# Kernel optimization log

Hardware: AMD Instinct MI355X
Metric: run time of the kernel (lower is better)

The kernel has to match this reference:

```python
import jax, jax.numpy as jnp
import numpy as np

N_NODES = 100000
N_EDGES = 3200000
N_GRAPHS = 256
FEAT = 128
HIDDEN = 128
N_CLASSES = 10


def setup_inputs() -> dict:
    key = jax.random.key(0)
    ks = jax.random.split(key, 12)
    x = jax.random.normal(ks[0], (N_NODES, FEAT), dtype=jnp.float32)
    edge_index = jax.random.randint(ks[1], (2, N_EDGES), 0, N_NODES, dtype=jnp.int64)
    batch = jnp.sort(jax.random.randint(ks[2], (N_NODES,), 0, N_GRAPHS, dtype=jnp.int64))
    s = 0.05
    return {
        "x": x,
        "edge_index": edge_index,
        "batch": batch,
        "W1": jax.random.normal(ks[3], (FEAT, HIDDEN), dtype=jnp.float32) * s,
        "b1": jnp.zeros((HIDDEN,), dtype=jnp.float32),
        "W2": jax.random.normal(ks[4], (HIDDEN, HIDDEN), dtype=jnp.float32) * s,
        "b2": jnp.zeros((HIDDEN,), dtype=jnp.float32),
        "W3": jax.random.normal(ks[5], (HIDDEN, HIDDEN), dtype=jnp.float32) * s,
        "b3": jnp.zeros((HIDDEN,), dtype=jnp.float32),
        "lin1_w": jax.random.normal(ks[6], (HIDDEN, HIDDEN), dtype=jnp.float32) * s,
        "lin1_b": jnp.zeros((HIDDEN,), dtype=jnp.float32),
        "lin2_w": jax.random.normal(ks[7], (HIDDEN, N_CLASSES), dtype=jnp.float32) * s,
        "lin2_b": jnp.zeros((N_CLASSES,), dtype=jnp.float32),
    }


def _gcn_norm(edge_index, n_nodes):
    # PyG GCNConv default: add self-loops, symmetric normalization.
    src = jnp.concatenate([edge_index[0], jnp.arange(n_nodes, dtype=edge_index.dtype)])
    dst = jnp.concatenate([edge_index[1], jnp.arange(n_nodes, dtype=edge_index.dtype)])
    deg = jax.ops.segment_sum(jnp.ones_like(dst, dtype=jnp.float32), dst, num_segments=n_nodes)
    dis = jnp.where(deg > 0, jax.lax.rsqrt(jnp.maximum(deg, 1.0)), 0.0)
    norm = dis[src] * dis[dst]  # [E + N]
    return src, dst, norm


def _gcn_conv(x, src, dst, norm, W, b, n_nodes):
    h = x @ W                               # [N, H]
    msg = h[src] * norm[:, None]            # gather + scale, [E+N, H]
    out = jax.ops.segment_sum(msg, dst, num_segments=n_nodes)  # scatter-add
    return out + b


def reference(x, edge_index, batch, W1, b1, W2, b2, W3, b3, lin1_w, lin1_b, lin2_w, lin2_b):
    n = x.shape[0]
    src, dst, norm = _gcn_norm(edge_index, n)
    h = jax.nn.relu(_gcn_conv(x, src, dst, norm, W1, b1, n))
    h = jax.nn.relu(_gcn_conv(h, src, dst, norm, W2, b2, n))
    h = jax.nn.relu(_gcn_conv(h, src, dst, norm, W3, b3, n))
    # global mean pool over graphs
    sums = jax.ops.segment_sum(h, batch, num_segments=N_GRAPHS)
    cnts = jax.ops.segment_sum(jnp.ones((n,), dtype=h.dtype), batch, num_segments=N_GRAPHS)
    g = sums / jnp.maximum(cnts, 1.0)[:, None]
    g = jax.nn.relu(g @ lin1_w + lin1_b)
    # dropout p=0.5 is identity at inference
    return g @ lin2_w + lin2_b
```

## Files before the change

### kernel.cpp

```cpp
#include <hip/hip_runtime.h>
#include <hip/hip_fp16.h>

#define FEAT 128
#define CHUNK 8192
#define BSH 7
#define CAP 6144
#define RSTRIDE 784

#define QS  16.0f
#define QSI 0.0625f

typedef _Float16 half8 __attribute__((ext_vector_type(8)));
typedef float floatx4 __attribute__((ext_vector_type(4)));
typedef float floatx2 __attribute__((ext_vector_type(2)));

__device__ __forceinline__ unsigned int enc8x4(float a, float b, float c, float d) {
  unsigned int r = __builtin_amdgcn_cvt_pk_fp8_f32(a, b, 0u, false);
  return __builtin_amdgcn_cvt_pk_fp8_f32(c, d, r, true);
}
__device__ __forceinline__ void acc8(unsigned int w, float* a) {
  floatx2 v0 = __builtin_amdgcn_cvt_pk_f32_fp8(w, false);
  floatx2 v1 = __builtin_amdgcn_cvt_pk_f32_fp8(w, true);
  a[0] += v0.x; a[1] += v0.y; a[2] += v1.x; a[3] += v1.y;
}


__global__ __launch_bounds__(256) void sort_prep_kernel(
    const int* __restrict__ ei, int E, int nchunks, int nbuk,
    int* __restrict__ pairs, int* __restrict__ runs,
    const float* __restrict__ W1, const float* __restrict__ W2,
    const float* __restrict__ W3, _Float16* __restrict__ P1,
    _Float16* __restrict__ P2, _Float16* __restrict__ P3,
    unsigned char* __restrict__ qA, unsigned char* __restrict__ qB, int N) {
  __shared__ int lhist[1024];
  __shared__ int lofs[1024];
  __shared__ int lcur[1024];
  __shared__ int tsum[256];
  __shared__ int stage[CHUNK];
  int t = threadIdx.x;
  if ((int)blockIdx.x >= nchunks) {
    int b = blockIdx.x - nchunks;
    if (b == 24) {
      if (t < 16) ((unsigned long long*)(qA + (size_t)N * FEAT))[t] = 0ull;
      else if (t < 32) ((unsigned long long*)(qB + (size_t)N * FEAT))[t - 16] = 0ull;
      return;
    }
    const float* W = (b < 8) ? W1 : (b < 16) ? W2 : W3;
    _Float16* P = (b < 8) ? P1 : (b < 16) ? P2 : P3;
    int e = (b & 7) * 256 + t;
    int l = e & 63;
    int ks = (e >> 6) & 3;
    int tn = e >> 8;
    int n = tn * 16 + (l & 15);
    int k0 = ks * 32 + (l >> 4) * 8;
    half8 v;
#pragma unroll
    for (int j = 0; j < 8; ++j) v[j] = (_Float16)W[(k0 + j) * 128 + n];
    *(half8*)(P + (size_t)e * 8) = v;
    return;
  }
  int c = blockIdx.x;
  int e0 = c * CHUNK;
  int e1 = e0 + CHUNK; if (e1 > E) e1 = E;
  int cnt = e1 - e0;
#pragma unroll
  for (int u = 0; u < 4; ++u) lhist[t + u * 256] = 0;
  __syncthreads();
  for (int j = e0 + t; j < e1; j += 256) atomicAdd(&lhist[ei[E + j] >> BSH], 1);
  __syncthreads();
  int a0 = lhist[4 * t], a1 = lhist[4 * t + 1];
  int a2 = lhist[4 * t + 2], a3 = lhist[4 * t + 3];
  int s = ((a0 + a1) + (a2 + a3));
  tsum[t] = s;
  __syncthreads();
  for (int o = 1; o < 256; o <<= 1) {
    int x = (t >= o) ? tsum[t - o] : 0;
    __syncthreads();
    tsum[t] += x;
    __syncthreads();
  }
  int base = tsum[t] - s;
  lofs[4 * t] = base;       lcur[4 * t] = base;
  lofs[4 * t + 1] = base + a0;           lcur[4 * t + 1] = base + a0;
  lofs[4 * t + 2] = base + a0 + a1;      lcur[4 * t + 2] = base + a0 + a1;
  lofs[4 * t + 3] = base + a0 + a1 + a2; lcur[4 * t + 3] = base + a0 + a1 + a2;
  __syncthreads();
  for (int k = t; k < nbuk; k += 256) runs[(size_t)c * RSTRIDE + k] = lofs[k];
  if (t == 0) runs[(size_t)c * RSTRIDE + nbuk] = cnt;
  for (int j = e0 + t; j < e1; j += 256) {
    int sv = ei[j];
    int d = ei[E + j];
    int p = atomicAdd(&lcur[d >> BSH], 1);
    stage[p] = sv | ((d & 127) << 24);
  }
  __syncthreads();
  for (int j = t; j < cnt; j += 256) pairs[e0 + j] = stage[j];
}

__global__ __launch_bounds__(256) void bucket_csr_kernel(
    const int* __restrict__ pairs, const int* __restrict__ runs, int nchunks,
    int nbuk, int2* __restrict__ row_se, float* __restrict__ dis,
    int* __restrict__ col, int N) {
  __shared__ int rs[512], rl[512], ro[512];
  __shared__ int cnt[128], sc[128];
  __shared__ int stage[CAP];
  int b = blockIdx.x, t = threadIdx.x;
  for (int c = t; c < 512; c += 256) {
    int s0 = 0, len = 0;
    if (c < nchunks) {
      const int* rr = runs + (size_t)c * RSTRIDE;
      s0 = rr[b];
      len = rr[b + 1] - s0;
    }
    rs[c] = s0; rl[c] = len;
  }
  if (t < 128) cnt[t] = 0;
  __syncthreads();
  ro[t] = rl[t]; ro[t + 256] = rl[t + 256];
  __syncthreads();
  for (int o = 1; o < 512; o <<= 1) {
    int v0 = (t >= o) ? ro[t - o] : 0;
    int v1 = (t + 256 >= o) ? ro[t + 256 - o] : 0;
    __syncthreads();
    ro[t] += v0; ro[t + 256] += v1;
    __syncthreads();
  }
  int ce = ro[511];
  int y0 = ro[t] - rl[t];
  int y1 = ro[t + 256] - rl[t + 256];
  __syncthreads();
  ro[t] = y0; ro[t + 256] = y1;
  __syncthreads();
  int colbase = b * CAP;
  bool fits = ce <= CAP;
  if (fits) {
    for (int c = t; c < nchunks; c += 256) {
      int gs = c * CHUNK + rs[c];
      int base = ro[c];
      int len = rl[c];
      for (int j = 0; j < len; ++j) {
        int p = pairs[gs + j];
        stage[base + j] = p;
        atomicAdd(&cnt[((unsigned)p) >> 24], 1);
      }
    }
  } else {
    for (int c = t; c < nchunks; c += 256) {
      int gs = c * CHUNK + rs[c];
      for (int j = 0; j < rl[c]; ++j)
        atomicAdd(&cnt[((unsigned)pairs[gs + j]) >> 24], 1);
    }
  }
  __syncthreads();
  int v = 0, excl = 0;
  if (t < 128) { v = cnt[t]; sc[t] = v; }
  __syncthreads();
  for (int o = 1; o < 128; o <<= 1) {
    int x = (t >= o && t < 128) ? sc[t - o] : 0;
    __syncthreads();
    if (t < 128) sc[t] += x;
    __syncthreads();
  }
  if (t < 128) {
    excl = sc[t] - v;
    int node = b * 128 + t;
    if (node < N) {
      row_se[node] = make_int2(colbase + excl, colbase + excl + v);
      dis[node] = rsqrtf((float)(v + 1));
    }
    cnt[t] = excl;
  }
  __syncthreads();
  if (fits) {
    for (int j = t; j < ce; j += 256) {
      int p = stage[j];
      int loc = atomicAdd(&cnt[((unsigned)p) >> 24], 1);
      col[colbase + loc] = (p & 0xFFFFFF) << 7;
    }
  } else {
    for (int c = t; c < nchunks; c += 256) {
      int gs = c * CHUNK + rs[c];
      for (int j = 0; j < rl[c]; ++j) {
        int p = pairs[gs + j];
        int loc = atomicAdd(&cnt[((unsigned)p) >> 24], 1);
        if (loc < CAP) col[colbase + loc] = (p & 0xFFFFFF) << 7;
      }
    }
  }
}


__global__ __launch_bounds__(256) void mm1_kernel(
    const float* __restrict__ Av, const _Float16* __restrict__ Wpk,
    const float* __restrict__ scale, unsigned char* __restrict__ C, int N) {
  int t = threadIdx.x;
  int wave = t >> 6, lane = t & 63;
  int quad = lane >> 4, nidx = lane & 15;
  int m0 = blockIdx.x * 64 + wave * 16;
  int arow = m0 + nidx;
  bool avalid = arow < N;
  floatx4 acc[8];
#pragma unroll
  for (int tn = 0; tn < 8; ++tn) acc[tn] = (floatx4){0.f, 0.f, 0.f, 0.f};
#pragma unroll
  for (int ks = 0; ks < 4; ++ks) {
    half8 x = {};
    if (avalid) {
      const float* p = Av + (size_t)arow * 128 + ks * 32 + quad * 8;
      float4 f0 = *(const float4*)p;
      float4 f1 = *(const float4*)(p + 4);
      x[0] = (_Float16)f0.x; x[1] = (_Float16)f0.y;
      x[2] = (_Float16)f0.z; x[3] = (_Float16)f0.w;
      x[4] = (_Float16)f1.x; x[5] = (_Float16)f1.y;
      x[6] = (_Float16)f1.z; x[7] = (_Float16)f1.w;
    }
#pragma unroll
    for (int tn = 0; tn < 8; ++tn) {
      half8 wfrag = *(const half8*)(Wpk + ((size_t)((tn * 4 + ks) * 64 + lane)) * 8);
      acc[tn] = __builtin_amdgcn_mfma_f32_16x16x32_f16(wfrag, x, acc[tn], 0, 0, 0);
    }
  }
  if (avalid) {
    float s = scale[arow] * QS;
#pragma unroll
    for (int tn = 0; tn < 8; ++tn) {
      unsigned int r = enc8x4(acc[tn][0] * s, acc[tn][1] * s,
                              acc[tn][2] * s, acc[tn][3] * s);
      *(unsigned int*)(C + (size_t)arow * 128 + tn * 16 + quad * 4) = r;
    }
  }
}

__global__ __launch_bounds__(256) void agg_fuse_kernel(
    const unsigned char* __restrict__ hs_in, const int2* __restrict__ row_se,
    const int* __restrict__ col, const float* __restrict__ dis,
    const float* __restrict__ bias, const _Float16* __restrict__ Wpk,
    unsigned char* __restrict__ hs_out, int N) {
  __shared__ _Float16 Xs[32][136];
  int t = threadIdx.x;
  int wave = t >> 6, lane = t & 63;
  int lin = lane & 7;
  int nl = wave * 8 + (lane >> 3);
  int node = blockIdx.x * 32 + nl;
  bool valid = node < N;
  int lin16 = lin * 16;
  int zoff = N << 7;
  float a[16];
#pragma unroll
  for (int j = 0; j < 16; ++j) a[j] = 0.f;
  int selfoff = (valid ? (node << 7) : zoff) + lin16;
  uint4 s0 = *(const uint4*)(hs_in + (unsigned)selfoff);
  acc8(s0.x, a); acc8(s0.y, a + 4); acc8(s0.z, a + 8); acc8(s0.w, a + 12);
  int2 se = valid ? row_se[node] : make_int2(0, 0);
  int i = se.x, e = se.y;
  while (__any(i < e)) {
    int c[8];
#pragma unroll
    for (int u = 0; u < 8; ++u) {
      int idx = i + u;
      c[u] = (idx < e) ? col[idx] : zoff;
    }
    uint4 r[8];
#pragma unroll
    for (int u = 0; u < 8; ++u)
      r[u] = *(const uint4*)(hs_in + (unsigned)(c[u] + lin16));
#pragma unroll
    for (int u = 0; u < 8; ++u) {
      acc8(r[u].x, a);     acc8(r[u].y, a + 4);
      acc8(r[u].z, a + 8); acc8(r[u].w, a + 12);
    }
    i += 8;
  }
  float d = valid ? dis[node] * QSI : 0.f;
  const float* bp = bias + lin16;
  half8 hx0, hx1;
#pragma unroll
  for (int j = 0; j < 8; ++j) {
    float o0 = valid ? fmaxf(fmaf(d, a[j], bp[j]), 0.f) : 0.f;
    float o1 = valid ? fmaxf(fmaf(d, a[j + 8], bp[j + 8]), 0.f) : 0.f;
    hx0[j] = (_Float16)o0;
    hx1[j] = (_Float16)o1;
  }
  *(half8*)&Xs[nl][lin16] = hx0;
  *(half8*)&Xs[nl][lin16 + 8] = hx1;
  __syncthreads();
  int quad = lane >> 4, nidx = lane & 15;
  int ntile = wave >> 1;
  int f0 = (wave & 1) * 4;
  floatx4 acc[4];
#pragma unroll
  for (int f = 0; f < 4; ++f) acc[f] = (floatx4){0.f, 0.f, 0.f, 0.f};
#pragma unroll
  for (int ks = 0; ks < 4; ++ks) {
    half8 x = *(const half8*)&Xs[ntile * 16 + nidx][ks * 32 + quad * 8];
#pragma unroll
    for (int f = 0; f < 4; ++f) {
      half8 wf = *(const half8*)(Wpk + ((size_t)(((f0 + f) * 4 + ks) * 64 + lane)) * 8);
      acc[f] = __builtin_amdgcn_mfma_f32_16x16x32_f16(wf, x, acc[f], 0, 0, 0);
    }
  }
  int onode = blockIdx.x * 32 + ntile * 16 + nidx;
  if (onode < N) {
    float sc = dis[onode] * QS;
#pragma unroll
    for (int f = 0; f < 4; ++f) {
      unsigned int rq = enc8x4(acc[f][0] * sc, acc[f][1] * sc,
                               acc[f][2] * sc, acc[f][3] * sc);
      *(unsigned int*)(hs_out + (size_t)onode * 128 + (f0 + f) * 16 + quad * 4) = rq;
    }
  }
}

__global__ __launch_bounds__(256) void agg_kernel(
    const unsigned char* __restrict__ hs, const int2* __restrict__ row_se,
    const int* __restrict__ col, const float* __restrict__ dis,
    const float* __restrict__ bias, _Float16* __restrict__ out, int N) {
  int t = threadIdx.x;
  int wave = t >> 6, lane = t & 63;
  int lin = lane & 7;
  int nl = wave * 8 + (lane >> 3);
  int node = blockIdx.x * 32 + nl;
  bool valid = node < N;
  int lin16 = lin * 16;
  int zoff = N << 7;
  float a[16];
#pragma unroll
  for (int j = 0; j < 16; ++j) a[j] = 0.f;
  int selfoff = (valid ? (node << 7) : zoff) + lin16;
  uint4 s0 = *(const uint4*)(hs + (unsigned)selfoff);
  acc8(s0.x, a); acc8(s0.y, a + 4); acc8(s0.z, a + 8); acc8(s0.w, a + 12);
  int2 se = valid ? row_se[node] : make_int2(0, 0);
  int i = se.x, e = se.y;
  while (__any(i < e)) {
    int c[8];
#pragma unroll
    for (int u = 0; u < 8; ++u) {
      int idx = i + u;
      c[u] = (idx < e) ? col[idx] : zoff;
    }
    uint4 r[8];
#pragma unroll
    for (int u = 0; u < 8; ++u)
      r[u] = *(const uint4*)(hs + (unsigned)(c[u] + lin16));
#pragma unroll
    for (int u = 0; u < 8; ++u) {
      acc8(r[u].x, a);     acc8(r[u].y, a + 4);
      acc8(r[u].z, a + 8); acc8(r[u].w, a + 12);
    }
    i += 8;
  }
  if (valid) {
    float d = dis[node] * QSI;
    const float* bp = bias + lin16;
    half8 hx0, hx1;
#pragma unroll
    for (int j = 0; j < 8; ++j) {
      hx0[j] = (_Float16)fmaxf(fmaf(d, a[j], bp[j]), 0.f);
      hx1[j] = (_Float16)fmaxf(fmaf(d, a[j + 8], bp[j + 8]), 0.f);
    }
    *(half8*)(out + (size_t)node * FEAT + lin16) = hx0;
    *(half8*)(out + (size_t)node * FEAT + lin16 + 8) = hx1;
  }
}

__global__ __launch_bounds__(128) void head_kernel(
    const __half* __restrict__ h, const int* __restrict__ batch,
    const float* __restrict__ l1w, const float* __restrict__ l1b,
    const float* __restrict__ l2w, const float* __restrict__ l2b,
    float* __restrict__ out, int N, int C) {
  __shared__ float row[128];
  __shared__ float row2[128];
  int grp = blockIdx.x, t = threadIdx.x;
  int lo = 0, hi = N;
  while (lo < hi) { int m = (lo + hi) >> 1; if (batch[m] < grp) lo = m + 1; else hi = m; }
  int start = lo;
  hi = N;
  while (lo < hi) { int m = (lo + hi) >> 1; if (batch[m] <= grp) lo = m + 1; else hi = m; }
  int end = lo;
  float a0 = 0.f, a1 = 0.f, a2 = 0.f, a3 = 0.f;
  int i = start;
  for (; i + 4 <= end; i += 4) {
    a0 += __half2float(h[(size_t)i * 128 + t]);
    a1 += __half2float(h[(size_t)(i + 1) * 128 + t]);
    a2 += __half2float(h[(size_t)(i + 2) * 128 + t]);
    a3 += __half2float(h[(size_t)(i + 3) * 128 + t]);
  }
  for (; i < end; ++i) a0 += __half2float(h[(size_t)i * 128 + t]);
  float sum = (a0 + a1) + (a2 + a3);
  float cntf = (float)(end - start);
  row[t] = sum / fmaxf(cntf, 1.0f);
  __syncthreads();
  float acc = l1b[t];
#pragma unroll 8
  for (int k = 0; k < 128; ++k) acc = fmaf(row[k], l1w[k * 128 + t], acc);
  row2[t] = fmaxf(acc, 0.f);
  __syncthreads();
  if (t < C) {
    float a = l2b[t];
#pragma unroll 8
    for (int k = 0; k < 128; ++k) a = fmaf(row2[k], l2w[k * C + t], a);
    out[grp * C + t] = a;
  }
}


extern "C" void kernel_launch(void* const* d_in, const int* in_sizes, int n_in,
                              void* d_out, int out_size, void* d_ws, size_t ws_size,
                              hipStream_t stream) {
  const float* x   = (const float*)d_in[0];
  const int*   ei  = (const int*)d_in[1];
  const int*   bat = (const int*)d_in[2];
  const float* W1  = (const float*)d_in[3];
  const float* b1  = (const float*)d_in[4];
  const float* W2  = (const float*)d_in[5];
  const float* b2  = (const float*)d_in[6];
  const float* W3  = (const float*)d_in[7];
  const float* b3  = (const float*)d_in[8];
  const float* l1w = (const float*)d_in[9];
  const float* l1b = (const float*)d_in[10];
  const float* l2w = (const float*)d_in[11];
  const float* l2b = (const float*)d_in[12];

  int N = in_sizes[2];
  int E = in_sizes[1] / 2;
  int C = in_sizes[12];
  int G = out_size / C;
  float* outp = (float*)d_out;

  char* wp = (char*)d_ws;
  auto alloc = [&](size_t bytes) -> void* {
    void* p = (void*)wp;
    wp += (bytes + 255) & ~(size_t)255;
    return p;
  };
  int nbuk    = (N + 127) / 128;
  int nchunks = (E + CHUNK - 1) / CHUNK;

  float*    dis    = (float*)alloc((size_t)N * 4);
  int2*     row_se = (int2*)alloc((size_t)N * 8);
  int*      col    = (int*)alloc((size_t)nbuk * CAP * 4);
  int*      pairs  = (int*)alloc((size_t)nchunks * CHUNK * 4);
  int*      runs   = (int*)alloc((size_t)nchunks * RSTRIDE * 4);
  _Float16* Wpk1   = (_Float16*)alloc(16384 * 2);
  _Float16* Wpk2   = (_Float16*)alloc(16384 * 2);
  _Float16* Wpk3   = (_Float16*)alloc(16384 * 2);
  unsigned char* qA = (unsigned char*)alloc((size_t)(N + 1) * FEAT);
  unsigned char* qB = (unsigned char*)alloc((size_t)(N + 1) * FEAT);
  _Float16* hout  = (_Float16*)alloc((size_t)N * FEAT * 2);

  sort_prep_kernel<<<nchunks + 25, 256, 0, stream>>>(
      ei, E, nchunks, nbuk, pairs, runs, W1, W2, W3, Wpk1, Wpk2, Wpk3,
      qA, qB, N);
  bucket_csr_kernel<<<nbuk, 256, 0, stream>>>(pairs, runs, nchunks, nbuk,
                                              row_se, dis, col, N);

  int mmB = (N + 63) / 64;
  int gB  = (N + 31) / 32;

  mm1_kernel<<<mmB, 256, 0, stream>>>(x, Wpk1, dis, qA, N);
  agg_fuse_kernel<<<gB, 256, 0, stream>>>(qA, row_se, col, dis, b1,
                                          Wpk2, qB, N);
  agg_fuse_kernel<<<gB, 256, 0, stream>>>(qB, row_se, col, dis, b2,
                                          Wpk3, qA, N);
  agg_kernel<<<gB, 256, 0, stream>>>(qA, row_se, col, dis, b3, hout, N);
  head_kernel<<<G, 128, 0, stream>>>((const __half*)hout, bat, l1w, l1b,
                                     l2w, l2b, outp, N, C);
}
```

Measured before the change: 470.0 us.

## Sort CSR neighbors by source range and sweep 128-node blocks in phases

The CSR build now counts edges per (destination, source-range) key, 16 source ranges per node, so each row's column list comes out grouped by source node range. The aggregation kernels now handle 128 nodes per block (4 per 8-lane group) and walk every node's neighbor list in 8 phases, in step with the other nodes. The block therefore touches roughly the same source range at the same time, which should improve L2 locality of the fp8 feature gathers. The cost is more shared-memory counters and scan work in the CSR build, more registers for four accumulators (capped at occupancy hint 3), and a smaller unroll (4 instead of 8) in the gather loop.

```diff
diff --git a/kernel.cpp b/kernel.cpp
--- a/kernel.cpp
+++ b/kernel.cpp
@@ -102,7 +102,8 @@
     int nbuk, int2* __restrict__ row_se, float* __restrict__ dis,
     int* __restrict__ col, int N) {
   __shared__ int rs[512], rl[512], ro[512];
-  __shared__ int cnt[128], sc[128];
+  __shared__ int cnt2[2048];
+  __shared__ int tsum[256];
   __shared__ int stage[CAP];
   int b = blockIdx.x, t = threadIdx.x;
   for (int c = t; c < 512; c += 256) {
@@ -114,7 +115,8 @@
     }
     rs[c] = s0; rl[c] = len;
   }
-  if (t < 128) cnt[t] = 0;
+#pragma unroll
+  for (int u = 0; u < 8; ++u) cnt2[t + u * 256] = 0;
   __syncthreads();
   ro[t] = rl[t]; ro[t + 256] = rl[t + 256];
   __syncthreads();
@@ -141,49 +143,66 @@
       for (int j = 0; j < len; ++j) {
         int p = pairs[gs + j];
         stage[base + j] = p;
-        atomicAdd(&cnt[((unsigned)p) >> 24], 1);
-      }
-    }
-  } else {
-    for (int c = t; c < nchunks; c += 256) {
-      int gs = c * CHUNK + rs[c];
-      for (int j = 0; j < rl[c]; ++j)
-        atomicAdd(&cnt[((unsigned)pairs[gs + j]) >> 24], 1);
-    }
-  }
-  __syncthreads();
-  int v = 0, excl = 0;
-  if (t < 128) { v = cnt[t]; sc[t] = v; }
-  __syncthreads();
-  for (int o = 1; o < 128; o <<= 1) {
-    int x = (t >= o && t < 128) ? sc[t - o] : 0;
-    __syncthreads();
-    if (t < 128) sc[t] += x;
-    __syncthreads();
-  }
-  if (t < 128) {
-    excl = sc[t] - v;
-    int node = b * 128 + t;
-    if (node < N) {
-      row_se[node] = make_int2(colbase + excl, colbase + excl + v);
-      dis[node] = rsqrtf((float)(v + 1));
-    }
-    cnt[t] = excl;
-  }
-  __syncthreads();
-  if (fits) {
-    for (int j = t; j < ce; j += 256) {
-      int p = stage[j];
-      int loc = atomicAdd(&cnt[((unsigned)p) >> 24], 1);
-      col[colbase + loc] = (p & 0xFFFFFF) << 7;
+        int key = (((unsigned)p) >> 24) * 16 + ((p & 0xFFFFFF) >> 13);
+        atomicAdd(&cnt2[key], 1);
+      }
     }
   } else {
     for (int c = t; c < nchunks; c += 256) {
       int gs = c * CHUNK + rs[c];
       for (int j = 0; j < rl[c]; ++j) {
         int p = pairs[gs + j];
-        int loc = atomicAdd(&cnt[((unsigned)p) >> 24], 1);
-        if (loc < CAP) col[colbase + loc] = (p & 0xFFFFFF) << 7;
+        int key = (((unsigned)p) >> 24) * 16 + ((p & 0xFFFFFF) >> 13);
+        atomicAdd(&cnt2[key], 1);
+      }
+    }
+  }
+  __syncthreads();
+  int av[8];
+#pragma unroll
+  for (int u = 0; u < 8; ++u) av[u] = cnt2[t * 8 + u];
+  int s = 0;
+#pragma unroll
+  for (int u = 0; u < 8; ++u) s += av[u];
+  tsum[t] = s;
+  __syncthreads();
+  for (int o = 1; o < 256; o <<= 1) {
+    int x = (t >= o) ? tsum[t - o] : 0;
+    __syncthreads();
+    tsum[t] += x;
+    __syncthreads();
+  }
+  int run = tsum[t] - s;
+#pragma unroll
+  for (int u = 0; u < 8; ++u) { int tmp = av[u]; cnt2[t * 8 + u] = run; run += tmp; }
+  __syncthreads();
+  if (t < 128) {
+    int startv = cnt2[t * 16];
+    int endv = (t == 127) ? ce : cnt2[t * 16 + 16];
+    int node = b * 128 + t;
+    if (node < N) {
+      row_se[node] = make_int2(colbase + startv, colbase + endv);
+      dis[node] = rsqrtf((float)(endv - startv + 1));
+    }
+  }
+  __syncthreads();
+  if (fits) {
+    for (int j = t; j < ce; j += 256) {
+      int p = stage[j];
+      int src = p & 0xFFFFFF;
+      int key = (((unsigned)p) >> 24) * 16 + (src >> 13);
+      int loc = atomicAdd(&cnt2[key], 1);
+      col[colbase + loc] = src << 7;
+    }
+  } else {
+    for (int c = t; c < nchunks; c += 256) {
+      int gs = c * CHUNK + rs[c];
+      for (int j = 0; j < rl[c]; ++j) {
+        int p = pairs[gs + j];
+        int src = p & 0xFFFFFF;
+        int key = (((unsigned)p) >> 24) * 16 + (src >> 13);
+        int loc = atomicAdd(&cnt2[key], 1);
+        if (loc < CAP) col[colbase + loc] = src << 7;
       }
     }
   }
@@ -231,135 +250,180 @@
   }
 }
 
-__global__ __launch_bounds__(256) void agg_fuse_kernel(
+__global__ __launch_bounds__(256, 3) void agg_fuse_kernel(
     const unsigned char* __restrict__ hs_in, const int2* __restrict__ row_se,
     const int* __restrict__ col, const float* __restrict__ dis,
     const float* __restrict__ bias, const _Float16* __restrict__ Wpk,
     unsigned char* __restrict__ hs_out, int N) {
-  __shared__ _Float16 Xs[32][136];
+  __shared__ _Float16 Xs[128][136];
   int t = threadIdx.x;
   int wave = t >> 6, lane = t & 63;
-  int lin = lane & 7;
-  int nl = wave * 8 + (lane >> 3);
-  int node = blockIdx.x * 32 + nl;
-  bool valid = node < N;
+  int g = t >> 3;
+  int lin = t & 7;
   int lin16 = lin * 16;
+  int nb = blockIdx.x * 128;
   int zoff = N << 7;
-  float a[16];
-#pragma unroll
-  for (int j = 0; j < 16; ++j) a[j] = 0.f;
-  int selfoff = (valid ? (node << 7) : zoff) + lin16;
-  uint4 s0 = *(const uint4*)(hs_in + (unsigned)selfoff);
-  acc8(s0.x, a); acc8(s0.y, a + 4); acc8(s0.z, a + 8); acc8(s0.w, a + 12);
-  int2 se = valid ? row_se[node] : make_int2(0, 0);
-  int i = se.x, e = se.y;
-  while (__any(i < e)) {
-    int c[8];
-#pragma unroll
-    for (int u = 0; u < 8; ++u) {
-      int idx = i + u;
-      c[u] = (idx < e) ? col[idx] : zoff;
-    }
-    uint4 r[8];
-#pragma unroll
-    for (int u = 0; u < 8; ++u)
-      r[u] = *(const uint4*)(hs_in + (unsigned)(c[u] + lin16));
-#pragma unroll
-    for (int u = 0; u < 8; ++u) {
-      acc8(r[u].x, a);     acc8(r[u].y, a + 4);
-      acc8(r[u].z, a + 8); acc8(r[u].w, a + 12);
-    }
-    i += 8;
-  }
-  float d = valid ? dis[node] * QSI : 0.f;
-  const float* bp = bias + lin16;
-  half8 hx0, hx1;
-#pragma unroll
-  for (int j = 0; j < 8; ++j) {
-    float o0 = valid ? fmaxf(fmaf(d, a[j], bp[j]), 0.f) : 0.f;
-    float o1 = valid ? fmaxf(fmaf(d, a[j + 8], bp[j + 8]), 0.f) : 0.f;
-    hx0[j] = (_Float16)o0;
-    hx1[j] = (_Float16)o1;
-  }
-  *(half8*)&Xs[nl][lin16] = hx0;
-  *(half8*)&Xs[nl][lin16 + 8] = hx1;
+  float a[4][16];
+#pragma unroll
+  for (int c = 0; c < 4; ++c)
+#pragma unroll
+    for (int j = 0; j < 16; ++j) a[c][j] = 0.f;
+  int ib[4], ie[4];
+#pragma unroll
+  for (int c = 0; c < 4; ++c) {
+    int node = nb + c * 32 + g;
+    bool valid = node < N;
+    int2 se = valid ? row_se[node] : make_int2(0, 0);
+    ib[c] = se.x; ie[c] = se.y;
+    int selfoff = (valid ? (node << 7) : zoff) + lin16;
+    uint4 s0 = *(const uint4*)(hs_in + (unsigned)selfoff);
+    acc8(s0.x, a[c]); acc8(s0.y, a[c] + 4);
+    acc8(s0.z, a[c] + 8); acc8(s0.w, a[c] + 12);
+  }
+#pragma unroll 1
+  for (int k = 0; k < 8; ++k) {
+#pragma unroll 1
+    for (int c = 0; c < 4; ++c) {
+      int d = ie[c] - ib[c];
+      int j  = ib[c] + ((k * d) >> 3);
+      int je = ib[c] + (((k + 1) * d) >> 3);
+      while (__any(j < je)) {
+        int cc[4];
+#pragma unroll
+        for (int u = 0; u < 4; ++u)
+          cc[u] = (j + u < je) ? col[j + u] : zoff;
+        uint4 rr[4];
+#pragma unroll
+        for (int u = 0; u < 4; ++u)
+          rr[u] = *(const uint4*)(hs_in + (unsigned)(cc[u] + lin16));
+#pragma unroll
+        for (int u = 0; u < 4; ++u) {
+          acc8(rr[u].x, a[c]);     acc8(rr[u].y, a[c] + 4);
+          acc8(rr[u].z, a[c] + 8); acc8(rr[u].w, a[c] + 12);
+        }
+        j += 4;
+      }
+    }
+  }
+  float bv[16];
+#pragma unroll
+  for (int j = 0; j < 16; ++j) bv[j] = bias[lin16 + j];
+#pragma unroll
+  for (int c = 0; c < 4; ++c) {
+    int node = nb + c * 32 + g;
+    bool valid = node < N;
+    float d = valid ? dis[node] * QSI : 0.f;
+    half8 hx0, hx1;
+#pragma unroll
+    for (int j = 0; j < 8; ++j) {
+      float o0 = valid ? fmaxf(fmaf(d, a[c][j], bv[j]), 0.f) : 0.f;
+      float o1 = valid ? fmaxf(fmaf(d, a[c][j + 8], bv[j + 8]), 0.f) : 0.f;
+      hx0[j] = (_Float16)o0;
+      hx1[j] = (_Float16)o1;
+    }
+    *(half8*)&Xs[c * 32 + g][lin16] = hx0;
+    *(half8*)&Xs[c * 32 + g][lin16 + 8] = hx1;
+  }
   __syncthreads();
   int quad = lane >> 4, nidx = lane & 15;
-  int ntile = wave >> 1;
   int f0 = (wave & 1) * 4;
-  floatx4 acc[4];
-#pragma unroll
-  for (int f = 0; f < 4; ++f) acc[f] = (floatx4){0.f, 0.f, 0.f, 0.f};
-#pragma unroll
-  for (int ks = 0; ks < 4; ++ks) {
-    half8 x = *(const half8*)&Xs[ntile * 16 + nidx][ks * 32 + quad * 8];
-#pragma unroll
-    for (int f = 0; f < 4; ++f) {
-      half8 wf = *(const half8*)(Wpk + ((size_t)(((f0 + f) * 4 + ks) * 64 + lane)) * 8);
-      acc[f] = __builtin_amdgcn_mfma_f32_16x16x32_f16(wf, x, acc[f], 0, 0, 0);
-    }
-  }
-  int onode = blockIdx.x * 32 + ntile * 16 + nidx;
-  if (onode < N) {
-    float sc = dis[onode] * QS;
-#pragma unroll
-    for (int f = 0; f < 4; ++f) {
-      unsigned int rq = enc8x4(acc[f][0] * sc, acc[f][1] * sc,
-                               acc[f][2] * sc, acc[f][3] * sc);
-      *(unsigned int*)(hs_out + (size_t)onode * 128 + (f0 + f) * 16 + quad * 4) = rq;
-    }
-  }
-}
-
-__global__ __launch_bounds__(256) void agg_kernel(
+#pragma unroll 1
+  for (int m = 0; m < 4; ++m) {
+    int ntile = (wave >> 1) + m * 2;
+    floatx4 acc4[4];
+#pragma unroll
+    for (int f = 0; f < 4; ++f) acc4[f] = (floatx4){0.f, 0.f, 0.f, 0.f};
+#pragma unroll
+    for (int ks = 0; ks < 4; ++ks) {
+      half8 x = *(const half8*)&Xs[ntile * 16 + nidx][ks * 32 + quad * 8];
+#pragma unroll
+      for (int f = 0; f < 4; ++f) {
+        half8 wf = *(const half8*)(Wpk + ((size_t)(((f0 + f) * 4 + ks) * 64 + lane)) * 8);
+        acc4[f] = __builtin_amdgcn_mfma_f32_16x16x32_f16(wf, x, acc4[f], 0, 0, 0);
+      }
+    }
+    int onode = nb + ntile * 16 + nidx;
+    if (onode < N) {
+      float sc = dis[onode] * QS;
+#pragma unroll
+      for (int f = 0; f < 4; ++f) {
+        unsigned int rq = enc8x4(acc4[f][0] * sc, acc4[f][1] * sc,
+                                 acc4[f][2] * sc, acc4[f][3] * sc);
+        *(unsigned int*)(hs_out + (size_t)onode * 128 + (f0 + f) * 16 + quad * 4) = rq;
+      }
+    }
+  }
+}
+
+__global__ __launch_bounds__(256, 3) void agg_kernel(
     const unsigned char* __restrict__ hs, const int2* __restrict__ row_se,
     const int* __restrict__ col, const float* __restrict__ dis,
     const float* __restrict__ bias, _Float16* __restrict__ out, int N) {
   int t = threadIdx.x;
-  int wave = t >> 6, lane = t & 63;
-  int lin = lane & 7;
-  int nl = wave * 8 + (lane >> 3);
-  int node = blockIdx.x * 32 + nl;
-  bool valid = node < N;
+  int g = t >> 3;
+  int lin = t & 7;
   int lin16 = lin * 16;
+  int nb = blockIdx.x * 128;
   int zoff = N << 7;
-  float a[16];
-#pragma unroll
-  for (int j = 0; j < 16; ++j) a[j] = 0.f;
-  int selfoff = (valid ? (node << 7) : zoff) + lin16;
-  uint4 s0 = *(const uint4*)(hs + (unsigned)selfoff);
-  acc8(s0.x, a); acc8(s0.y, a + 4); acc8(s0.z, a + 8); acc8(s0.w, a + 12);
-  int2 se = valid ? row_se[node] : make_int2(0, 0);
-  int i = se.x, e = se.y;
-  while (__any(i < e)) {
-    int c[8];
-#pragma unroll
-    for (int u = 0; u < 8; ++u) {
-      int idx = i + u;
-      c[u] = (idx < e) ? col[idx] : zoff;
-    }
-    uint4 r[8];
-#pragma unroll
-    for (int u = 0; u < 8; ++u)
-      r[u] = *(const uint4*)(hs + (unsigned)(c[u] + lin16));
-#pragma unroll
-    for (int u = 0; u < 8; ++u) {
-      acc8(r[u].x, a);     acc8(r[u].y, a + 4);
-      acc8(r[u].z, a + 8); acc8(r[u].w, a + 12);
-    }
-    i += 8;
-  }
-  if (valid) {
-    float d = dis[node] * QSI;
-    const float* bp = bias + lin16;
-    half8 hx0, hx1;
-#pragma unroll
-    for (int j = 0; j < 8; ++j) {
-      hx0[j] = (_Float16)fmaxf(fmaf(d, a[j], bp[j]), 0.f);
-      hx1[j] = (_Float16)fmaxf(fmaf(d, a[j + 8], bp[j + 8]), 0.f);
-    }
-    *(half8*)(out + (size_t)node * FEAT + lin16) = hx0;
-    *(half8*)(out + (size_t)node * FEAT + lin16 + 8) = hx1;
+  float a[4][16];
+#pragma unroll
+  for (int c = 0; c < 4; ++c)
+#pragma unroll
+    for (int j = 0; j < 16; ++j) a[c][j] = 0.f;
+  int ib[4], ie[4];
+#pragma unroll
+  for (int c = 0; c < 4; ++c) {
+    int node = nb + c * 32 + g;
+    bool valid = node < N;
+    int2 se = valid ? row_se[node] : make_int2(0, 0);
+    ib[c] = se.x; ie[c] = se.y;
+    int selfoff = (valid ? (node << 7) : zoff) + lin16;
+    uint4 s0 = *(const uint4*)(hs + (unsigned)selfoff);
+    acc8(s0.x, a[c]); acc8(s0.y, a[c] + 4);
+    acc8(s0.z, a[c] + 8); acc8(s0.w, a[c] + 12);
+  }
+#pragma unroll 1
+  for (int k = 0; k < 8; ++k) {
+#pragma unroll 1
+    for (int c = 0; c < 4; ++c) {
+      int d = ie[c] - ib[c];
+      int j  = ib[c] + ((k * d) >> 3);
+      int je = ib[c] + (((k + 1) * d) >> 3);
+      while (__any(j < je)) {
+        int cc[4];
+#pragma unroll
+        for (int u = 0; u < 4; ++u)
+          cc[u] = (j + u < je) ? col[j + u] : zoff;
+        uint4 rr[4];
+#pragma unroll
+        for (int u = 0; u < 4; ++u)
+          rr[u] = *(const uint4*)(hs + (unsigned)(cc[u] + lin16));
+#pragma unroll
+        for (int u = 0; u < 4; ++u) {
+          acc8(rr[u].x, a[c]);     acc8(rr[u].y, a[c] + 4);
+          acc8(rr[u].z, a[c] + 8); acc8(rr[u].w, a[c] + 12);
+        }
+        j += 4;
+      }
+    }
+  }
+  float bv[16];
+#pragma unroll
+  for (int j = 0; j < 16; ++j) bv[j] = bias[lin16 + j];
+#pragma unroll
+  for (int c = 0; c < 4; ++c) {
+    int node = nb + c * 32 + g;
+    if (node < N) {
+      float d = dis[node] * QSI;
+      half8 hx0, hx1;
+#pragma unroll
+      for (int j = 0; j < 8; ++j) {
+        hx0[j] = (_Float16)fmaxf(fmaf(d, a[c][j], bv[j]), 0.f);
+        hx1[j] = (_Float16)fmaxf(fmaf(d, a[c][j + 8], bv[j + 8]), 0.f);
+      }
+      *(half8*)(out + (size_t)node * FEAT + lin16) = hx0;
+      *(half8*)(out + (size_t)node * FEAT + lin16 + 8) = hx1;
+    }
   }
 }
 
@@ -455,14 +519,13 @@
                                               row_se, dis, col, N);
 
   int mmB = (N + 63) / 64;
-  int gB  = (N + 31) / 32;
 
   mm1_kernel<<<mmB, 256, 0, stream>>>(x, Wpk1, dis, qA, N);
-  agg_fuse_kernel<<<gB, 256, 0, stream>>>(qA, row_se, col, dis, b1,
-                                          Wpk2, qB, N);
-  agg_fuse_kernel<<<gB, 256, 0, stream>>>(qB, row_se, col, dis, b2,
-                                          Wpk3, qA, N);
-  agg_kernel<<<gB, 256, 0, stream>>>(qA, row_se, col, dis, b3, hout, N);
+  agg_fuse_kernel<<<nbuk, 256, 0, stream>>>(qA, row_se, col, dis, b1,
+                                            Wpk2, qB, N);
+  agg_fuse_kernel<<<nbuk, 256, 0, stream>>>(qB, row_se, col, dis, b2,
+                                            Wpk3, qA, N);
+  agg_kernel<<<nbuk, 256, 0, stream>>>(qA, row_se, col, dis, b3, hout, N);
   head_kernel<<<G, 128, 0, stream>>>((const __half*)hout, bat, l1w, l1b,
                                      l2w, l2b, outp, N, C);
 }
```

Measured after the change: 1.143 ms. +143.3%, slower.

## Fuse global mean-pool sums into final aggregation kernel via atomics

Applied to the files above, without the earlier changes.

The last aggregation kernel now stages each block's 32 activated node rows in shared memory and does a segmented sum by graph id. It atomically adds the partial sums into a per-graph float accumulator, which is zeroed in an extra prep block. The head kernel reads these sums instead of rescanning a full half-precision activation buffer. This removes the write and reread of the N×128 activation tensor, at the cost of a block-level sync, global float atomics, and order-dependent float summation.

```diff
diff --git a/kernel.cpp b/kernel.cpp
--- a/kernel.cpp
+++ b/kernel.cpp
@@ -31,7 +31,8 @@
     const float* __restrict__ W1, const float* __restrict__ W2,
     const float* __restrict__ W3, _Float16* __restrict__ P1,
     _Float16* __restrict__ P2, _Float16* __restrict__ P3,
-    unsigned char* __restrict__ qA, unsigned char* __restrict__ qB, int N) {
+    unsigned char* __restrict__ qA, unsigned char* __restrict__ qB,
+    float* __restrict__ gsum, int G, int N) {
   __shared__ int lhist[1024];
   __shared__ int lofs[1024];
   __shared__ int lcur[1024];
@@ -43,6 +44,11 @@
     if (b == 24) {
       if (t < 16) ((unsigned long long*)(qA + (size_t)N * FEAT))[t] = 0ull;
       else if (t < 32) ((unsigned long long*)(qB + (size_t)N * FEAT))[t - 16] = 0ull;
+      return;
+    }
+    if (b == 25) {
+      float4 z = {0.f, 0.f, 0.f, 0.f};
+      for (int i = t; i < G * 32; i += 256) ((float4*)gsum)[i] = z;
       return;
     }
     const float* W = (b < 8) ? W1 : (b < 16) ? W2 : W3;
@@ -311,10 +317,13 @@
   }
 }
 
-__global__ __launch_bounds__(256) void agg_kernel(
+__global__ __launch_bounds__(256) void agg_pool_kernel(
     const unsigned char* __restrict__ hs, const int2* __restrict__ row_se,
     const int* __restrict__ col, const float* __restrict__ dis,
-    const float* __restrict__ bias, _Float16* __restrict__ out, int N) {
+    const float* __restrict__ bias, const int* __restrict__ batch,
+    float* __restrict__ gsum, int N) {
+  __shared__ float Hs[32][132];
+  __shared__ int ig[32];
   int t = threadIdx.x;
   int wave = t >> 6, lane = t & 63;
   int lin = lane & 7;
@@ -349,22 +358,32 @@
     }
     i += 8;
   }
-  if (valid) {
-    float d = dis[node] * QSI;
-    const float* bp = bias + lin16;
-    half8 hx0, hx1;
-#pragma unroll
-    for (int j = 0; j < 8; ++j) {
-      hx0[j] = (_Float16)fmaxf(fmaf(d, a[j], bp[j]), 0.f);
-      hx1[j] = (_Float16)fmaxf(fmaf(d, a[j + 8], bp[j + 8]), 0.f);
-    }
-    *(half8*)(out + (size_t)node * FEAT + lin16) = hx0;
-    *(half8*)(out + (size_t)node * FEAT + lin16 + 8) = hx1;
+  float d = valid ? dis[node] * QSI : 0.f;
+  const float* bp = bias + lin16;
+#pragma unroll
+  for (int j = 0; j < 16; ++j)
+    Hs[nl][lin16 + j] = valid ? fmaxf(fmaf(d, a[j], bp[j]), 0.f) : 0.f;
+  if (lin == 0) ig[nl] = batch[valid ? node : (N - 1)];
+  __syncthreads();
+  if (t < 128) {
+    float run = 0.f;
+    int cur = ig[0];
+#pragma unroll 4
+    for (int n = 0; n < 32; ++n) {
+      int g2 = ig[n];
+      if (g2 != cur) {
+        atomicAdd(&gsum[cur * 128 + t], run);
+        run = 0.f;
+        cur = g2;
+      }
+      run += Hs[n][t];
+    }
+    atomicAdd(&gsum[cur * 128 + t], run);
   }
 }
 
 __global__ __launch_bounds__(128) void head_kernel(
-    const __half* __restrict__ h, const int* __restrict__ batch,
+    const float* __restrict__ gsum, const int* __restrict__ batch,
     const float* __restrict__ l1w, const float* __restrict__ l1b,
     const float* __restrict__ l2w, const float* __restrict__ l2b,
     float* __restrict__ out, int N, int C) {
@@ -377,18 +396,8 @@
   hi = N;
   while (lo < hi) { int m = (lo + hi) >> 1; if (batch[m] <= grp) lo = m + 1; else hi = m; }
   int end = lo;
-  float a0 = 0.f, a1 = 0.f, a2 = 0.f, a3 = 0.f;
-  int i = start;
-  for (; i + 4 <= end; i += 4) {
-    a0 += __half2float(h[(size_t)i * 128 + t]);
-    a1 += __half2float(h[(size_t)(i + 1) * 128 + t]);
-    a2 += __half2float(h[(size_t)(i + 2) * 128 + t]);
-    a3 += __half2float(h[(size_t)(i + 3) * 128 + t]);
-  }
-  for (; i < end; ++i) a0 += __half2float(h[(size_t)i * 128 + t]);
-  float sum = (a0 + a1) + (a2 + a3);
   float cntf = (float)(end - start);
-  row[t] = sum / fmaxf(cntf, 1.0f);
+  row[t] = gsum[grp * 128 + t] / fmaxf(cntf, 1.0f);
   __syncthreads();
   float acc = l1b[t];
 #pragma unroll 8
@@ -446,11 +455,11 @@
   _Float16* Wpk3   = (_Float16*)alloc(16384 * 2);
   unsigned char* qA = (unsigned char*)alloc((size_t)(N + 1) * FEAT);
   unsigned char* qB = (unsigned char*)alloc((size_t)(N + 1) * FEAT);
-  _Float16* hout  = (_Float16*)alloc((size_t)N * FEAT * 2);
-
-  sort_prep_kernel<<<nchunks + 25, 256, 0, stream>>>(
+  float*    gsum   = (float*)alloc((size_t)G * FEAT * 4);
+
+  sort_prep_kernel<<<nchunks + 26, 256, 0, stream>>>(
       ei, E, nchunks, nbuk, pairs, runs, W1, W2, W3, Wpk1, Wpk2, Wpk3,
-      qA, qB, N);
+      qA, qB, gsum, G, N);
   bucket_csr_kernel<<<nbuk, 256, 0, stream>>>(pairs, runs, nchunks, nbuk,
                                               row_se, dis, col, N);
 
@@ -462,7 +471,7 @@
                                           Wpk2, qB, N);
   agg_fuse_kernel<<<gB, 256, 0, stream>>>(qB, row_se, col, dis, b2,
                                           Wpk3, qA, N);
-  agg_kernel<<<gB, 256, 0, stream>>>(qA, row_se, col, dis, b3, hout, N);
-  head_kernel<<<G, 128, 0, stream>>>((const __half*)hout, bat, l1w, l1b,
-                                     l2w, l2b, outp, N, C);
-}
+  agg_pool_kernel<<<gB, 256, 0, stream>>>(qA, row_se, col, dis, b3, bat,
+                                          gsum, N);
+  head_kernel<<<G, 128, 0, stream>>>(gsum, bat, l1w, l1b, l2w, l2b, outp, N, C);
+}
```

Result: faster. 443.5 us (-5.6%).
